# Kernel tuning notes

Hardware: AMD Instinct MI355X
Metric: run time of the kernel (lower is better)

Reference implementation:

```python
import jax, jax.numpy as jnp
import numpy as np

EMBED = 512
HEADS = 8
HD = EMBED // HEADS  # 64
LAYERS = 4
VOCAB = 16
SDIM = 3
TDEPTH = 8
BATCH = 2
SEQ = 1024
FF = 4 * EMBED
EPS = 1e-6      # fast-transformers CausalLinearAttention eps
LN_EPS = 1e-5   # torch LayerNorm default


def layer_norm(x, g, b):
    m = jnp.mean(x, axis=-1, keepdims=True)
    v = jnp.mean((x - m) ** 2, axis=-1, keepdims=True)
    return (x - m) * jax.lax.rsqrt(v + LN_EPS) * g + b


def setup_inputs() -> dict:
    key = jax.random.key(0)
    ks = iter(jax.random.split(key, 64))
    def nrm(shape, scale=0.02):
        return jax.random.normal(next(ks), shape, jnp.float32) * scale
    inp = {}
    inp['value'] = jax.random.randint(next(ks), (BATCH, SEQ), 0, VOCAB + 1)
    inp['depth'] = jax.random.randint(next(ks), (BATCH, SEQ), 0, TDEPTH + 1)
    inp['pos'] = jax.random.randint(next(ks), (SDIM, BATCH, SEQ), 0, 2 ** TDEPTH + 1)
    inp['sos'] = jax.random.normal(next(ks), (EMBED,), jnp.float32)
    # embeddings with padding_idx=0 -> zero row 0
    inp['tok_emb'] = nrm((VOCAB + 1, EMBED), 1.0).at[0].set(0.0)
    inp['depth_emb'] = nrm((TDEPTH + 1, EMBED), 1.0).at[0].set(0.0)
    inp['spatial_emb'] = nrm((SDIM, 2 ** TDEPTH + 1, EMBED), 1.0).at[:, 0].set(0.0)
    # per-layer stacked params (weights stored [in, out])
    for nm in ('Wq', 'Wk', 'Wv', 'Wo'):
        inp[nm] = nrm((LAYERS, EMBED, EMBED))
    for nm in ('bq', 'bk', 'bv', 'bo'):
        inp[nm] = jnp.zeros((LAYERS, EMBED), jnp.float32)
    inp['ln1_g'] = jnp.ones((LAYERS, EMBED), jnp.float32)
    inp['ln1_b'] = jnp.zeros((LAYERS, EMBED), jnp.float32)
    inp['ln2_g'] = jnp.ones((LAYERS, EMBED), jnp.float32)
    inp['ln2_b'] = jnp.zeros((LAYERS, EMBED), jnp.float32)
    inp['W1'] = nrm((LAYERS, EMBED, FF))
    inp['b1'] = jnp.zeros((LAYERS, FF), jnp.float32)
    inp['W2'] = nrm((LAYERS, FF, EMBED))
    inp['b2'] = jnp.zeros((LAYERS, EMBED), jnp.float32)
    inp['lnf_g'] = jnp.ones((EMBED,), jnp.float32)
    inp['lnf_b'] = jnp.zeros((EMBED,), jnp.float32)
    inp['Wh'] = nrm((EMBED, VOCAB + 1))
    return inp


def reference(value, depth, pos, sos, tok_emb, depth_emb, spatial_emb,
              Wq, bq, Wk, bk, Wv, bv, Wo, bo,
              ln1_g, ln1_b, ln2_g, ln2_b, W1, b1, W2, b2,
              lnf_g, lnf_b, Wh):
    N, S = value.shape
    # embedding sum
    x = tok_emb[value] + depth_emb[depth]
    for a in range(SDIM):
        x = x + spatial_emb[a][pos[a]]
    # shift right, prepend SOS
    x = jnp.concatenate([jnp.broadcast_to(sos, (N, 1, EMBED)), x[:, :-1, :]], axis=1)
    kmask = (value != 0).astype(x.dtype)  # (N,S) length mask applied to keys
    for i in range(LAYERS):
        # causal-linear attention (elu+1 feature map)
        q = jax.nn.elu((x @ Wq[i] + bq[i]).reshape(N, S, HEADS, HD)) + 1.0
        k = jax.nn.elu((x @ Wk[i] + bk[i]).reshape(N, S, HEADS, HD)) + 1.0
        v = (x @ Wv[i] + bv[i]).reshape(N, S, HEADS, HD)
        k = k * kmask[:, :, None, None]
        kv = jnp.cumsum(jnp.einsum('nshd,nshm->nshdm', k, v), axis=1)  # prefix K^T V state
        num = jnp.einsum('nshd,nshdm->nshm', q, kv)
        z = 1.0 / (jnp.einsum('nshd,nshd->nsh', q, jnp.cumsum(k, axis=1)) + EPS)
        attn = (num * z[..., None]).reshape(N, S, EMBED) @ Wo[i] + bo[i]
        # post-norm transformer block (fast-transformers TransformerEncoderLayer)
        x = layer_norm(x + attn, ln1_g[i], ln1_b[i])
        y = jax.nn.gelu(x @ W1[i] + b1[i], approximate=False) @ W2[i] + b2[i]
        x = layer_norm(x + y, ln2_g[i], ln2_b[i])
    x = layer_norm(x, lnf_g, lnf_b)  # encoder final norm
    return x @ Wh  # (N, S, num_vocab+1)
```

## Files before the change

kernel.cpp:

```cpp
#include <hip/hip_runtime.h>
#include <math.h>

#define EMB 512
#define SEQL 1024
#define NBATCH 2
#define NHEAD 8
#define FFDIM 2048
#define NLAYER 4
#define NROWS (NBATCH*SEQL)
#define CHUNK 128
#define NCH (SEQL/CHUNK)
#define QSTR 1536
#define LN_EPS_F 1e-5f
#define ATT_EPS_F 1e-6f

typedef __bf16 bf16x8 __attribute__((ext_vector_type(8)));
typedef float f32x4 __attribute__((ext_vector_type(4)));

__device__ __forceinline__ unsigned short f2bf(float f) {
    unsigned int u = __float_as_uint(f);
    u += 0x7FFFu + ((u >> 16) & 1u);
    return (unsigned short)(u >> 16);
}
__device__ __forceinline__ float bf2f(unsigned short x) {
    return __uint_as_float(((unsigned int)x) << 16);
}
__device__ __forceinline__ void gl_lds16(const unsigned short* g, unsigned short* l) {
    __builtin_amdgcn_global_load_lds(
        (__attribute__((address_space(1))) void*)const_cast<unsigned short*>(g),
        (__attribute__((address_space(3))) void*)l, 16, 0, 0);
}

__global__ void k_embed(const int* __restrict__ value, const int* __restrict__ depth,
                        const int* __restrict__ pos, const float* __restrict__ sos,
                        const float* __restrict__ tok, const float* __restrict__ dep,
                        const float* __restrict__ spa, float* __restrict__ X,
                        unsigned short* __restrict__ Xb) {
    int row = blockIdx.x;
    int n = row / SEQL, s = row % SEQL;
    int e = threadIdx.x * 4;
    float4 o;
    if (s == 0) {
        o = *(const float4*)(sos + e);
    } else {
        int sp = s - 1;
        int tv = value[n*SEQL + sp];
        int dv = depth[n*SEQL + sp];
        float4 a = *(const float4*)(tok + (size_t)tv*EMB + e);
        float4 b = *(const float4*)(dep + (size_t)dv*EMB + e);
        o.x = a.x+b.x; o.y = a.y+b.y; o.z = a.z+b.z; o.w = a.w+b.w;
#pragma unroll
        for (int ax = 0; ax < 3; ++ax) {
            int p = pos[((size_t)ax*NBATCH + n)*SEQL + sp];
            float4 c = *(const float4*)(spa + ((size_t)ax*257 + p)*EMB + e);
            o.x += c.x; o.y += c.y; o.z += c.z; o.w += c.w;
        }
    }
    *(float4*)(X + (size_t)row*EMB + e) = o;
    ushort4 ob; ob.x = f2bf(o.x); ob.y = f2bf(o.y); ob.z = f2bf(o.z); ob.w = f2bf(o.w);
    *(ushort4*)(Xb + (size_t)row*EMB + e) = ob;
}

__global__ __launch_bounds__(256) void k_wconv(
        const float* __restrict__ Wq0, const float* __restrict__ Wk0, const float* __restrict__ Wv0,
        const float* __restrict__ Wo0, const float* __restrict__ W10, const float* __restrict__ W20,
        const float* __restrict__ bq0, const float* __restrict__ bk0, const float* __restrict__ bv0,
        unsigned short* __restrict__ wAll, float* __restrict__ bqkv) {
    int idx = blockIdx.x*256 + threadIdx.x;
    if (idx >= 1572864) {
        int t = idx - 1572864;
        if (t < 6144) {
            int L = t / 1536, c = t % 1536;
            float v = (c < 512) ? bq0[L*512 + c] : (c < 1024) ? bk0[L*512 + c - 512] : bv0[L*512 + c - 1024];
            bqkv[L*1536 + c] = v;
        }
        return;
    }
    int L = idx / 393216;
    int t0 = idx % 393216;
    const float* Wq = Wq0 + (size_t)L*EMB*EMB;
    const float* Wk = Wk0 + (size_t)L*EMB*EMB;
    const float* Wv = Wv0 + (size_t)L*EMB*EMB;
    const float* Wo = Wo0 + (size_t)L*EMB*EMB;
    const float* W1 = W10 + (size_t)L*EMB*FFDIM;
    const float* W2 = W20 + (size_t)L*FFDIM*EMB;
    unsigned short* lay = wAll + (size_t)L*3145728;
    unsigned short* qkvT = lay;
    unsigned short* woT  = lay + 786432;
    unsigned short* w1T  = lay + 1048576;
    unsigned short* w2T  = lay + 2097152;

    const float* src; unsigned short* dst; size_t soff; size_t doff;
    if (t0 < 131072) {
        int sub = t0 >> 15, t = t0 & 32767;
        int kb = t >> 9, n = t & 511;
        src = (sub == 0) ? Wq : (sub == 1) ? Wk : (sub == 2) ? Wv : Wo;
        soff = (size_t)kb*8*512 + n;
        if (sub < 3) { dst = qkvT; doff = ((size_t)kb*1536 + sub*512 + n)*8; }
        else         { dst = woT;  doff = ((size_t)kb*512 + n)*8; }
        unsigned int p[4];
#pragma unroll
        for (int t2 = 0; t2 < 4; ++t2) {
            unsigned int lo = f2bf(src[soff + (size_t)(2*t2)*512]);
            unsigned int hi = f2bf(src[soff + (size_t)(2*t2+1)*512]);
            p[t2] = lo | (hi << 16);
        }
        *(uint4*)(dst + doff) = make_uint4(p[0], p[1], p[2], p[3]);
    } else if (t0 < 262144) {
        int t = t0 - 131072;
        int kb = t >> 11, n = t & 2047;
        soff = (size_t)kb*8*2048 + n;
        doff = ((size_t)kb*2048 + n)*8;
        unsigned int p[4];
#pragma unroll
        for (int t2 = 0; t2 < 4; ++t2) {
            unsigned int lo = f2bf(W1[soff + (size_t)(2*t2)*2048]);
            unsigned int hi = f2bf(W1[soff + (size_t)(2*t2+1)*2048]);
            p[t2] = lo | (hi << 16);
        }
        *(uint4*)(w1T + doff) = make_uint4(p[0], p[1], p[2], p[3]);
    } else {
        int t = t0 - 262144;
        int kb = t >> 9, n = t & 511;
        soff = (size_t)kb*8*512 + n;
        doff = ((size_t)kb*512 + n)*8;
        unsigned int p[4];
#pragma unroll
        for (int t2 = 0; t2 < 4; ++t2) {
            unsigned int lo = f2bf(W2[soff + (size_t)(2*t2)*512]);
            unsigned int hi = f2bf(W2[soff + (size_t)(2*t2+1)*512]);
            p[t2] = lo | (hi << 16);
        }
        *(uint4*)(w2T + doff) = make_uint4(p[0], p[1], p[2], p[3]);
    }
}

template<int BM, int BN, int WR, int WC, int ACT, int KS>
__global__ __launch_bounds__(WR*WC*64) void k_mgemm(
        const unsigned short* __restrict__ A, const unsigned short* __restrict__ Wt,
        const float* __restrict__ bias, const int* __restrict__ maskv,
        float* __restrict__ Cf, unsigned short* __restrict__ Cb,
        int N, int K, int lda, int ldc) {
    constexpr int THREADS = WR*WC*64;
    constexpr int WM = BM/WR, WN = BN/WC;
    constexpr int FM = WM/16, FN = WN/16;
    __shared__ __align__(16) unsigned short As[BM*32];
    __shared__ __align__(16) unsigned short Bs[BN*32];
    int tid = threadIdx.x;
    int lane = tid & 63;
    int l15 = lane & 15, lg = lane >> 4;
    int wid = tid >> 6;
    int wm = (wid / WC) * WM, wn = (wid % WC) * WN;
    int bm = blockIdx.y * BM, bn = blockIdx.x * BN;
    int kz = blockIdx.z;
    int ksl = K / KS;
    int kbeg = kz * ksl, kend = kbeg + ksl;

    f32x4 acc[FM][FN] = {};

    int a_off = (wm + l15)*32 + lg*8;
    int b_off = lg*BN*8 + (wn + l15)*8;

    for (int k0 = kbeg; k0 < kend; k0 += 32) {
#pragma unroll
        for (int i = 0; i < BM*4/THREADS; ++i) {
            int s = tid + i*THREADS;
            int m = s >> 2, kq = s & 3;
            gl_lds16(A + (size_t)(bm + m)*lda + k0 + kq*8, &As[s*8]);
        }
#pragma unroll
        for (int i = 0; i < BN*4/THREADS; ++i) {
            int s = tid + i*THREADS;
            int kb = s / BN, n = s - kb*BN;
            gl_lds16(Wt + ((size_t)(k0/8 + kb)*N + bn + n)*8, &Bs[s*8]);
        }
        __syncthreads();
        bf16x8 af[FM], bfr[FN];
#pragma unroll
        for (int mi = 0; mi < FM; ++mi) af[mi] = *(const bf16x8*)&As[a_off + mi*512];
#pragma unroll
        for (int ni = 0; ni < FN; ++ni) bfr[ni] = *(const bf16x8*)&Bs[b_off + ni*128];
#pragma unroll
        for (int mi = 0; mi < FM; ++mi)
#pragma unroll
            for (int ni = 0; ni < FN; ++ni)
                acc[mi][ni] = __builtin_amdgcn_mfma_f32_16x16x32_bf16(af[mi], bfr[ni], acc[mi][ni], 0, 0, 0);
        __syncthreads();
    }

    int r0 = bm + wm + lg*4;
    int c0 = bn + wn + l15;
    float* Cfz = Cf + (size_t)kz * 1048576;
#pragma unroll
    for (int mi = 0; mi < FM; ++mi) {
#pragma unroll
        for (int ni = 0; ni < FN; ++ni) {
            int col = c0 + ni*16;
#pragma unroll
            for (int j = 0; j < 4; ++j) {
                int row = r0 + mi*16 + j;
                float c = acc[mi][ni][j];
                if (KS == 1 || kz == 0) c += bias[col];
                if (ACT == 4) {
                    int reg = col >> 9;
                    if (reg == 0) { c = (c > 0.f) ? c + 1.f : expf(c); }
                    else if (reg == 1) { c = (c > 0.f) ? c + 1.f : expf(c); c *= (maskv[row] != 0) ? 1.f : 0.f; }
                    Cb[(size_t)row*ldc + col] = f2bf(c);
                } else if (ACT == 3) {
                    c = 0.5f * c * (1.f + erff(c * 0.70710678118654752f));
                    Cb[(size_t)row*ldc + col] = f2bf(c);
                } else {
                    Cfz[(size_t)row*ldc + col] = c;
                }
            }
        }
    }
}

__global__ __launch_bounds__(256) void k_cpart(
        const unsigned short* __restrict__ QKVb, float* __restrict__ Mpart, float* __restrict__ Upart) {
    int b = blockIdx.x;
    int c = b % NCH, h = (b / NCH) % NHEAD, n = b / (NCH * NHEAD);
    const unsigned short* Kp = QKVb + (size_t)(n*SEQL + c*CHUNK)*QSTR + 512 + h*64;
    const unsigned short* Vp = Kp + 512;
    __shared__ float Ks[8][64], Vs[8][64];
    int tid = threadIdx.x;
    int dk = tid >> 2, dv0 = (tid & 3) * 16;
    int lr = tid >> 5, lc = (tid & 31) * 2;
    float acc[16] = {};
    float uacc = 0.f;
    for (int s0 = 0; s0 < CHUNK; s0 += 8) {
        ushort2 k2 = *(const ushort2*)(Kp + (size_t)(s0 + lr)*QSTR + lc);
        ushort2 v2 = *(const ushort2*)(Vp + (size_t)(s0 + lr)*QSTR + lc);
        Ks[lr][lc] = bf2f(k2.x); Ks[lr][lc+1] = bf2f(k2.y);
        Vs[lr][lc] = bf2f(v2.x); Vs[lr][lc+1] = bf2f(v2.y);
        __syncthreads();
#pragma unroll
        for (int ss = 0; ss < 8; ++ss) {
            float kk = Ks[ss][dk];
#pragma unroll
            for (int j = 0; j < 16; ++j) acc[j] += kk * Vs[ss][dv0 + j];
        }
        if (tid < 64) {
#pragma unroll
            for (int ss = 0; ss < 8; ++ss) uacc += Ks[ss][tid];
        }
        __syncthreads();
    }
    size_t base = ((size_t)(n*NHEAD + h)*NCH + c) * 4096;
#pragma unroll
    for (int j = 0; j < 16; ++j) Mpart[base + (size_t)dk*64 + dv0 + j] = acc[j];
    if (tid < 64) Upart[((size_t)(n*NHEAD + h)*NCH + c)*64 + tid] = uacc;
}

__global__ __launch_bounds__(512) void k_cattend(
        const unsigned short* __restrict__ QKVb, const float* __restrict__ Mpart,
        const float* __restrict__ Upart, unsigned short* __restrict__ Ab) {
    int b = blockIdx.x;
    int c = b % NCH, h = (b / NCH) % NHEAD, n = b / (NCH * NHEAD);
    int nh = n*NHEAD + h;
    int tid = threadIdx.x;
    int wid = tid >> 6, lane = tid & 63;
    int l15 = lane & 15, lg = lane >> 4;
    __shared__ __align__(16) unsigned short Vt[64*200];
    __shared__ __align__(16) unsigned short St[11264];
    __shared__ float wf[64];
    int rowbase = n*SEQL + c*CHUNK;

    {
        int j = tid & 127, vd0 = (tid >> 7) * 16;
        const unsigned short* vp = QKVb + (size_t)(rowbase + j)*QSTR + 1024 + h*64 + vd0;
        uint4 u0 = *(const uint4*)vp;
        uint4 u1 = *(const uint4*)(vp + 8);
        const unsigned short* e0 = (const unsigned short*)&u0;
        const unsigned short* e1 = (const unsigned short*)&u1;
#pragma unroll
        for (int t = 0; t < 8; ++t) Vt[(vd0 + t)*200 + j] = e0[t];
#pragma unroll
        for (int t = 0; t < 8; ++t) Vt[(vd0 + 8 + t)*200 + j] = e1[t];
    }
    {
        int d = tid & 63, vd0 = (tid >> 6) * 8;
        float pr[8] = {};
        for (int cc = 0; cc < c; ++cc) {
            const float* pp = Mpart + ((size_t)nh*NCH + cc)*4096 + (size_t)d*64 + vd0;
            float4 p0 = *(const float4*)pp;
            float4 p1 = *(const float4*)(pp + 4);
            pr[0]+=p0.x; pr[1]+=p0.y; pr[2]+=p0.z; pr[3]+=p0.w;
            pr[4]+=p1.x; pr[5]+=p1.y; pr[6]+=p1.z; pr[7]+=p1.w;
        }
#pragma unroll
        for (int t = 0; t < 8; ++t) Vt[(vd0 + t)*200 + 128 + d] = f2bf(pr[t]);
    }
    if (tid < 64) {
        float u = 0.f;
        for (int cc = 0; cc < c; ++cc) u += Upart[((size_t)nh*NCH + cc)*64 + tid];
        wf[tid] = u;
    }

    int r0 = wid * 16;
    int koff = lg * 8;
    const unsigned short* qp = QKVb + (size_t)(rowbase + r0 + l15)*QSTR + h*64 + koff;
    uint4 uq0 = *(const uint4*)qp;
    uint4 uq1 = *(const uint4*)(qp + 32);
    bf16x8 aq0 = *(bf16x8*)&uq0;
    bf16x8 aq1 = *(bf16x8*)&uq1;

    int nact = (wid & ~1) + 2;
    int sstr_ = 32*((wid >> 1) + 1) + 8;
    int p_ = wid >> 1;
    int sig = p_*(p_+1) + (wid & 1)*(p_+1);
    int stoff_ = 128*wid + 512*sig;

    float rsum[4] = {0.f, 0.f, 0.f, 0.f};
    for (int nt = 0; nt < nact; ++nt) {
        int j0 = nt*16;
        const unsigned short* kp = QKVb + (size_t)(rowbase + j0 + l15)*QSTR + 512 + h*64 + koff;
        uint4 uk0 = *(const uint4*)kp;
        uint4 uk1 = *(const uint4*)(kp + 32);
        f32x4 s = {0.f, 0.f, 0.f, 0.f};
        s = __builtin_amdgcn_mfma_f32_16x16x32_bf16(aq0, *(bf16x8*)&uk0, s, 0, 0, 0);
        s = __builtin_amdgcn_mfma_f32_16x16x32_bf16(aq1, *(bf16x8*)&uk1, s, 0, 0, 0);
        int jcol = j0 + l15;
#pragma unroll
        for (int r = 0; r < 4; ++r) {
            int irow = r0 + lg*4 + r;
            float sv = (jcol <= irow) ? s[r] : 0.f;
            rsum[r] += sv;
            St[stoff_ + (lg*4 + r)*sstr_ + jcol] = f2bf(sv);
        }
    }
    __syncthreads();

    float qw = 0.f;
    const unsigned short* q0e = (const unsigned short*)&uq0;
    const unsigned short* q1e = (const unsigned short*)&uq1;
#pragma unroll
    for (int jj = 0; jj < 8; ++jj) {
        qw += bf2f(q0e[jj]) * wf[koff + jj];
        qw += bf2f(q1e[jj]) * wf[32 + koff + jj];
    }
    qw += __shfl_xor(qw, 16);
    qw += __shfl_xor(qw, 32);

    f32x4 o[4] = {};
    int nkr = (wid >> 1) + 1;
    for (int ks = 0; ks < nkr; ++ks) {
        bf16x8 as = *(bf16x8*)&St[stoff_ + l15*sstr_ + ks*32 + koff];
#pragma unroll
        for (int nt = 0; nt < 4; ++nt) {
            bf16x8 bv = *(bf16x8*)&Vt[(nt*16 + l15)*200 + ks*32 + koff];
            o[nt] = __builtin_amdgcn_mfma_f32_16x16x32_bf16(as, bv, o[nt], 0, 0, 0);
        }
    }
#pragma unroll
    for (int kk = 0; kk < 2; ++kk) {
        bf16x8 as = kk ? aq1 : aq0;
#pragma unroll
        for (int nt = 0; nt < 4; ++nt) {
            bf16x8 bv = *(bf16x8*)&Vt[(nt*16 + l15)*200 + 128 + kk*32 + koff];
            o[nt] = __builtin_amdgcn_mfma_f32_16x16x32_bf16(as, bv, o[nt], 0, 0, 0);
        }
    }

#pragma unroll
    for (int r = 0; r < 4; ++r) {
        float v = rsum[r];
        v += __shfl_xor(v, 1); v += __shfl_xor(v, 2);
        v += __shfl_xor(v, 4); v += __shfl_xor(v, 8);
        rsum[r] = v;
    }
#pragma unroll
    for (int r = 0; r < 4; ++r) {
        float qwr = __shfl(qw, lg*4 + r);
        float z = 1.f / (rsum[r] + qwr + ATT_EPS_F);
        int orow = rowbase + r0 + lg*4 + r;
        unsigned short* op = Ab + (size_t)orow*EMB + h*64 + l15;
#pragma unroll
        for (int nt = 0; nt < 4; ++nt)
            op[nt*16] = f2bf(o[nt][r] * z);
    }
}

__global__ __launch_bounds__(256) void k_ln(
        const float* __restrict__ X, const float* __restrict__ R, int nsl,
        const float* __restrict__ g, const float* __restrict__ bb,
        float* __restrict__ Y, unsigned short* __restrict__ Yb) {
    int row = blockIdx.x, tid = threadIdx.x;
    float2 v = *(const float2*)(X + (size_t)row*EMB + tid*2);
    for (int z = 0; z < nsl; ++z) {
        float2 r = *(const float2*)(R + (size_t)z*1048576 + (size_t)row*EMB + tid*2);
        v.x += r.x; v.y += r.y;
    }
    float s = v.x + v.y, ss = v.x*v.x + v.y*v.y;
#pragma unroll
    for (int off = 32; off; off >>= 1) {
        s  += __shfl_down(s, off);
        ss += __shfl_down(ss, off);
    }
    __shared__ float sb[4], ssb[4];
    int wid = tid >> 6, lane = tid & 63;
    if (!lane) { sb[wid] = s; ssb[wid] = ss; }
    __syncthreads();
    float tot  = sb[0] + sb[1] + sb[2] + sb[3];
    float tots = ssb[0] + ssb[1] + ssb[2] + ssb[3];
    float mean = tot * (1.f/EMB);
    float var  = tots * (1.f/EMB) - mean*mean;
    float inv  = rsqrtf(var + LN_EPS_F);
    int e = tid*2;
    float2 o;
    o.x = (v.x - mean)*inv*g[e]   + bb[e];
    o.y = (v.y - mean)*inv*g[e+1] + bb[e+1];
    *(float2*)(Y + (size_t)row*EMB + e) = o;
    ushort2 ob; ob.x = f2bf(o.x); ob.y = f2bf(o.y);
    *(ushort2*)(Yb + (size_t)row*EMB + e) = ob;
}

__global__ __launch_bounds__(256) void k_lnhead(
        const float* __restrict__ X, const float* __restrict__ g, const float* __restrict__ bb,
        const float* __restrict__ Wh, float* __restrict__ out) {
    __shared__ float ys[8][512];
    __shared__ float whs[512*17];
    int tid = threadIdx.x;
    for (int i = tid; i < 512*17; i += 256) whs[i] = Wh[i];

    int row = tid >> 5, l32 = tid & 31;
    int rg = blockIdx.x * 8 + row;
    const float* xr = X + (size_t)rg*EMB + l32*16;
    float v[16];
    float s = 0.f, ss = 0.f;
#pragma unroll
    for (int i = 0; i < 4; ++i) {
        float4 a = *(const float4*)(xr + i*4);
        v[i*4+0]=a.x; v[i*4+1]=a.y; v[i*4+2]=a.z; v[i*4+3]=a.w;
        s += a.x+a.y+a.z+a.w;
        ss += a.x*a.x+a.y*a.y+a.z*a.z+a.w*a.w;
    }
#pragma unroll
    for (int off = 1; off < 32; off <<= 1) { s += __shfl_xor(s, off); ss += __shfl_xor(ss, off); }
    float mean = s * (1.f/EMB);
    float var  = ss * (1.f/EMB) - mean*mean;
    float inv  = rsqrtf(var + LN_EPS_F);
    int c0 = l32*16;
#pragma unroll
    for (int i = 0; i < 16; ++i) {
        float y = (v[i] - mean)*inv*g[c0+i] + bb[c0+i];
        ys[row][c0+i] = y;
    }
    __syncthreads();

    float part[17];
#pragma unroll
    for (int cc = 0; cc < 17; ++cc) part[cc] = 0.f;
    for (int kk = 0; kk < 16; ++kk) {
        int k = c0 + kk;
        float yv = ys[row][k];
#pragma unroll
        for (int cc = 0; cc < 17; ++cc) part[cc] += yv * whs[k*17 + cc];
    }
#pragma unroll
    for (int cc = 0; cc < 17; ++cc) {
        float pv = part[cc];
#pragma unroll
        for (int off = 1; off < 32; off <<= 1) pv += __shfl_xor(pv, off);
        if (l32 == 0) out[(size_t)rg*17 + cc] = pv;
    }
}

extern "C" void kernel_launch(void* const* d_in, const int* in_sizes, int n_in,
                              void* d_out, int out_size, void* d_ws, size_t ws_size,
                              hipStream_t stream) {
    (void)in_sizes; (void)n_in; (void)out_size; (void)ws_size;
    const int*   value = (const int*)d_in[0];
    const int*   depth = (const int*)d_in[1];
    const int*   pos   = (const int*)d_in[2];
    const float* sos   = (const float*)d_in[3];
    const float* tok   = (const float*)d_in[4];
    const float* dep   = (const float*)d_in[5];
    const float* spa   = (const float*)d_in[6];
    const float* Wq0   = (const float*)d_in[7];
    const float* Wk0   = (const float*)d_in[8];
    const float* Wv0   = (const float*)d_in[9];
    const float* Wo0   = (const float*)d_in[10];
    const float* bq0   = (const float*)d_in[11];
    const float* bk0   = (const float*)d_in[12];
    const float* bv0   = (const float*)d_in[13];
    const float* bo0   = (const float*)d_in[14];
    const float* ln1g  = (const float*)d_in[15];
    const float* ln1b  = (const float*)d_in[16];
    const float* ln2g  = (const float*)d_in[17];
    const float* ln2b  = (const float*)d_in[18];
    const float* W10   = (const float*)d_in[19];
    const float* b10   = (const float*)d_in[20];
    const float* W20   = (const float*)d_in[21];
    const float* b20   = (const float*)d_in[22];
    const float* lnfg  = (const float*)d_in[23];
    const float* lnfb  = (const float*)d_in[24];
    const float* Wh    = (const float*)d_in[25];
    float* out = (float*)d_out;
    float* ws  = (float*)d_ws;

    float*          X     = ws;
    unsigned short* Xb    = (unsigned short*)(ws + 1048576);
    unsigned short* QKVb  = (unsigned short*)(ws + 1572864);
    unsigned short* Ab    = (unsigned short*)(ws + 3145728);
    unsigned short* Hb    = (unsigned short*)(ws + 1572864);
    float*          Mpart = ws + 3670016;
    float*          Upart = ws + 4194304;
    float*          AO    = ws + 4202496;
    float*          bqkv  = ws + 8396800;
    unsigned short* wAll  = (unsigned short*)(ws + 8402944);

    k_embed<<<NROWS, 128, 0, stream>>>(value, depth, pos, sos, tok, dep, spa, X, Xb);
    k_wconv<<<6168, 256, 0, stream>>>(Wq0, Wk0, Wv0, Wo0, W10, W20, bq0, bk0, bv0, wAll, bqkv);

    for (int L = 0; L < NLAYER; ++L) {
        unsigned short* lay  = wAll + (size_t)L*3145728;
        unsigned short* qkvT = lay;
        unsigned short* woT  = lay + 786432;
        unsigned short* w1T  = lay + 1048576;
        unsigned short* w2T  = lay + 2097152;

        k_mgemm<64,128,2,2,4,1><<<dim3(12,32), 256, 0, stream>>>(
            Xb, qkvT, bqkv + L*1536, value, nullptr, QKVb, 1536, 512, 512, 1536);

        k_cpart<<<NBATCH*NHEAD*NCH, 256, 0, stream>>>(QKVb, Mpart, Upart);
        k_cattend<<<NBATCH*NHEAD*NCH, 512, 0, stream>>>(QKVb, Mpart, Upart, Ab);

        k_mgemm<64,64,2,2,0,2><<<dim3(8,32,2), 256, 0, stream>>>(
            Ab, woT, bo0 + (size_t)L*EMB, nullptr, AO, nullptr, 512, 512, 512, 512);
        k_ln<<<NROWS, 256, 0, stream>>>(X, AO, 2, ln1g + (size_t)L*EMB, ln1b + (size_t)L*EMB, X, Xb);

        k_mgemm<64,128,2,2,3,1><<<dim3(16,32), 256, 0, stream>>>(
            Xb, w1T, b10 + (size_t)L*FFDIM, nullptr, nullptr, Hb, 2048, 512, 512, 2048);

        k_mgemm<64,64,2,2,0,4><<<dim3(8,32,4), 256, 0, stream>>>(
            Hb, w2T, b20 + (size_t)L*EMB, nullptr, AO, nullptr, 512, 2048, 2048, 512);
        k_ln<<<NROWS, 256, 0, stream>>>(X, AO, 4, ln2g + (size_t)L*EMB, ln2b + (size_t)L*EMB, X, Xb);
    }
    k_lnhead<<<NROWS/8, 256, 0, stream>>>(X, lnfg, lnfb, Wh, out);
}
```

Measured before the change: 424.4 us.

## Split chunked linear-attention kernels into two blocks per chunk for more parallelism

Both the chunk-partial kernel and the attend kernel now launch twice as many blocks. The partial kernel splits each 128-row chunk into two 64-row halves, and the attend kernel splits its 8 waves into two 256-thread blocks of 4 waves each. With only 128 blocks before, the GPU's compute units were underused. In exchange, each attend block redundantly loads the full V tile and sums twice as many prefix partials, Mpart and Upart grow, and the workspace offsets shift to fit.

```diff
diff --git a/kernel.cpp b/kernel.cpp
--- a/kernel.cpp
+++ b/kernel.cpp
@@ -220,8 +220,12 @@
 __global__ __launch_bounds__(256) void k_cpart(
         const unsigned short* __restrict__ QKVb, float* __restrict__ Mpart, float* __restrict__ Upart) {
     int b = blockIdx.x;
-    int c = b % NCH, h = (b / NCH) % NHEAD, n = b / (NCH * NHEAD);
-    const unsigned short* Kp = QKVb + (size_t)(n*SEQL + c*CHUNK)*QSTR + 512 + h*64;
+    int half = b & 1;
+    int cidx = b >> 1;
+    int c = cidx % NCH;
+    int nh = cidx / NCH;
+    int h = nh % NHEAD, n = nh / NHEAD;
+    const unsigned short* Kp = QKVb + (size_t)(n*SEQL + c*CHUNK + half*64)*QSTR + 512 + h*64;
     const unsigned short* Vp = Kp + 512;
     __shared__ float Ks[8][64], Vs[8][64];
     int tid = threadIdx.x;
@@ -229,7 +233,7 @@
     int lr = tid >> 5, lc = (tid & 31) * 2;
     float acc[16] = {};
     float uacc = 0.f;
-    for (int s0 = 0; s0 < CHUNK; s0 += 8) {
+    for (int s0 = 0; s0 < 64; s0 += 8) {
         ushort2 k2 = *(const ushort2*)(Kp + (size_t)(s0 + lr)*QSTR + lc);
         ushort2 v2 = *(const ushort2*)(Vp + (size_t)(s0 + lr)*QSTR + lc);
         Ks[lr][lc] = bf2f(k2.x); Ks[lr][lc+1] = bf2f(k2.y);
@@ -247,20 +251,24 @@
         }
         __syncthreads();
     }
-    size_t base = ((size_t)(n*NHEAD + h)*NCH + c) * 4096;
+    size_t base = (size_t)b * 4096;
 #pragma unroll
     for (int j = 0; j < 16; ++j) Mpart[base + (size_t)dk*64 + dv0 + j] = acc[j];
-    if (tid < 64) Upart[((size_t)(n*NHEAD + h)*NCH + c)*64 + tid] = uacc;
-}
-
-__global__ __launch_bounds__(512) void k_cattend(
+    if (tid < 64) Upart[(size_t)b*64 + tid] = uacc;
+}
+
+__global__ __launch_bounds__(256) void k_cattend(
         const unsigned short* __restrict__ QKVb, const float* __restrict__ Mpart,
         const float* __restrict__ Upart, unsigned short* __restrict__ Ab) {
     int b = blockIdx.x;
-    int c = b % NCH, h = (b / NCH) % NHEAD, n = b / (NCH * NHEAD);
-    int nh = n*NHEAD + h;
+    int grp = b & 1;
+    int cidx = b >> 1;
+    int c = cidx % NCH;
+    int nh = cidx / NCH;
+    int h = nh % NHEAD, n = nh / NHEAD;
     int tid = threadIdx.x;
-    int wid = tid >> 6, lane = tid & 63;
+    int wid = (grp << 2) + (tid >> 6);
+    int lane = tid & 63;
     int l15 = lane & 15, lg = lane >> 4;
     __shared__ __align__(16) unsigned short Vt[64*200];
     __shared__ __align__(16) unsigned short St[11264];
@@ -268,33 +276,41 @@
     int rowbase = n*SEQL + c*CHUNK;
 
     {
-        int j = tid & 127, vd0 = (tid >> 7) * 16;
-        const unsigned short* vp = QKVb + (size_t)(rowbase + j)*QSTR + 1024 + h*64 + vd0;
-        uint4 u0 = *(const uint4*)vp;
-        uint4 u1 = *(const uint4*)(vp + 8);
-        const unsigned short* e0 = (const unsigned short*)&u0;
-        const unsigned short* e1 = (const unsigned short*)&u1;
-#pragma unroll
-        for (int t = 0; t < 8; ++t) Vt[(vd0 + t)*200 + j] = e0[t];
-#pragma unroll
-        for (int t = 0; t < 8; ++t) Vt[(vd0 + 8 + t)*200 + j] = e1[t];
+        int j = tid & 127;
+        const unsigned short* vp = QKVb + (size_t)(rowbase + j)*QSTR + 1024 + h*64;
+#pragma unroll
+        for (int vh = 0; vh < 2; ++vh) {
+            int vd0 = (tid >> 7) * 16 + vh * 32;
+            uint4 u0 = *(const uint4*)(vp + vd0);
+            uint4 u1 = *(const uint4*)(vp + vd0 + 8);
+            const unsigned short* e0 = (const unsigned short*)&u0;
+            const unsigned short* e1 = (const unsigned short*)&u1;
+#pragma unroll
+            for (int t = 0; t < 8; ++t) Vt[(vd0 + t)*200 + j] = e0[t];
+#pragma unroll
+            for (int t = 0; t < 8; ++t) Vt[(vd0 + 8 + t)*200 + j] = e1[t];
+        }
     }
     {
-        int d = tid & 63, vd0 = (tid >> 6) * 8;
-        float pr[8] = {};
-        for (int cc = 0; cc < c; ++cc) {
-            const float* pp = Mpart + ((size_t)nh*NCH + cc)*4096 + (size_t)d*64 + vd0;
-            float4 p0 = *(const float4*)pp;
-            float4 p1 = *(const float4*)(pp + 4);
-            pr[0]+=p0.x; pr[1]+=p0.y; pr[2]+=p0.z; pr[3]+=p0.w;
-            pr[4]+=p1.x; pr[5]+=p1.y; pr[6]+=p1.z; pr[7]+=p1.w;
-        }
-#pragma unroll
-        for (int t = 0; t < 8; ++t) Vt[(vd0 + t)*200 + 128 + d] = f2bf(pr[t]);
+        int d = tid & 63;
+#pragma unroll
+        for (int ph = 0; ph < 2; ++ph) {
+            int vd0 = (tid >> 6) * 8 + ph * 32;
+            float pr[8] = {};
+            for (int p = 0; p < 2*c; ++p) {
+                const float* pp = Mpart + ((size_t)nh*NCH*2 + p)*4096 + (size_t)d*64 + vd0;
+                float4 p0 = *(const float4*)pp;
+                float4 p1 = *(const float4*)(pp + 4);
+                pr[0]+=p0.x; pr[1]+=p0.y; pr[2]+=p0.z; pr[3]+=p0.w;
+                pr[4]+=p1.x; pr[5]+=p1.y; pr[6]+=p1.z; pr[7]+=p1.w;
+            }
+#pragma unroll
+            for (int t = 0; t < 8; ++t) Vt[(vd0 + t)*200 + 128 + d] = f2bf(pr[t]);
+        }
     }
     if (tid < 64) {
         float u = 0.f;
-        for (int cc = 0; cc < c; ++cc) u += Upart[((size_t)nh*NCH + cc)*64 + tid];
+        for (int p = 0; p < 2*c; ++p) u += Upart[((size_t)nh*NCH*2 + p)*64 + tid];
         wf[tid] = u;
     }
 
@@ -506,10 +522,10 @@
     unsigned short* Ab    = (unsigned short*)(ws + 3145728);
     unsigned short* Hb    = (unsigned short*)(ws + 1572864);
     float*          Mpart = ws + 3670016;
-    float*          Upart = ws + 4194304;
-    float*          AO    = ws + 4202496;
-    float*          bqkv  = ws + 8396800;
-    unsigned short* wAll  = (unsigned short*)(ws + 8402944);
+    float*          Upart = ws + 4718592;
+    float*          AO    = ws + 4734976;
+    float*          bqkv  = ws + 8929280;
+    unsigned short* wAll  = (unsigned short*)(ws + 8935424);
 
     k_embed<<<NROWS, 128, 0, stream>>>(value, depth, pos, sos, tok, dep, spa, X, Xb);
     k_wconv<<<6168, 256, 0, stream>>>(Wq0, Wk0, Wv0, Wo0, W10, W20, bq0, bk0, bv0, wAll, bqkv);
@@ -524,8 +540,8 @@
         k_mgemm<64,128,2,2,4,1><<<dim3(12,32), 256, 0, stream>>>(
             Xb, qkvT, bqkv + L*1536, value, nullptr, QKVb, 1536, 512, 512, 1536);
 
-        k_cpart<<<NBATCH*NHEAD*NCH, 256, 0, stream>>>(QKVb, Mpart, Upart);
-        k_cattend<<<NBATCH*NHEAD*NCH, 512, 0, stream>>>(QKVb, Mpart, Upart, Ab);
+        k_cpart<<<NBATCH*NHEAD*NCH*2, 256, 0, stream>>>(QKVb, Mpart, Upart);
+        k_cattend<<<NBATCH*NHEAD*NCH*2, 256, 0, stream>>>(QKVb, Mpart, Upart, Ab);
 
         k_mgemm<64,64,2,2,0,2><<<dim3(8,32,2), 256, 0, stream>>>(
             Ab, woT, bo0 + (size_t)L*EMB, nullptr, AO, nullptr, 512, 512, 512, 512);
```

After: 430.6 us. Within noise of the previous version (+1.5%).

## Triple-buffer GEMM LDS tiles with async global-to-LDS prefetch pipeline

Applied to the files above, without the earlier changes.

Reworks the MFMA GEMM main loop into a three-stage software pipeline. Two K-tiles ahead are issued with global_load_lds into rotating LDS buffers, and explicit vmcnt waits plus raw s_barrier replace the __syncthreads pairs. The goal is to hide global memory latency behind MFMA compute. It triples LDS usage, which may lower occupancy, and it depends on hand-counted vmcnt values that only work for certain NL values and assume nt >= 2.

```diff
diff --git a/kernel.cpp b/kernel.cpp
--- a/kernel.cpp
+++ b/kernel.cpp
@@ -29,6 +29,13 @@
     __builtin_amdgcn_global_load_lds(
         (__attribute__((address_space(1))) void*)const_cast<unsigned short*>(g),
         (__attribute__((address_space(3))) void*)l, 16, 0, 0);
+}
+template<int N_> __device__ __forceinline__ void wait_vm() {
+    if constexpr (N_ == 0) asm volatile("s_waitcnt vmcnt(0)" ::: "memory");
+    else if constexpr (N_ == 2) asm volatile("s_waitcnt vmcnt(2)" ::: "memory");
+    else if constexpr (N_ == 3) asm volatile("s_waitcnt vmcnt(3)" ::: "memory");
+    else if constexpr (N_ == 4) asm volatile("s_waitcnt vmcnt(4)" ::: "memory");
+    else if constexpr (N_ == 6) asm volatile("s_waitcnt vmcnt(6)" ::: "memory");
 }
 
 __global__ void k_embed(const int* __restrict__ value, const int* __restrict__ depth,
@@ -144,8 +151,11 @@
     constexpr int THREADS = WR*WC*64;
     constexpr int WM = BM/WR, WN = BN/WC;
     constexpr int FM = WM/16, FN = WN/16;
-    __shared__ __align__(16) unsigned short As[BM*32];
-    __shared__ __align__(16) unsigned short Bs[BN*32];
+    constexpr int AL = BM*4/THREADS;
+    constexpr int BL = BN*4/THREADS;
+    constexpr int NL = AL + BL;
+    __shared__ __align__(16) unsigned short As[3][BM*32];
+    __shared__ __align__(16) unsigned short Bs[3][BN*32];
     int tid = threadIdx.x;
     int lane = tid & 63;
     int l15 = lane & 15, lg = lane >> 4;
@@ -154,39 +164,63 @@
     int bm = blockIdx.y * BM, bn = blockIdx.x * BN;
     int kz = blockIdx.z;
     int ksl = K / KS;
-    int kbeg = kz * ksl, kend = kbeg + ksl;
+    int kbeg = kz * ksl;
+    int nt = ksl / 32;
 
     f32x4 acc[FM][FN] = {};
 
     int a_off = (wm + l15)*32 + lg*8;
     int b_off = lg*BN*8 + (wn + l15)*8;
 
-    for (int k0 = kbeg; k0 < kend; k0 += 32) {
-#pragma unroll
-        for (int i = 0; i < BM*4/THREADS; ++i) {
+    auto stage = [&](int buf, int ks) {
+        int k0 = kbeg + ks*32;
+#pragma unroll
+        for (int i = 0; i < AL; ++i) {
             int s = tid + i*THREADS;
             int m = s >> 2, kq = s & 3;
-            gl_lds16(A + (size_t)(bm + m)*lda + k0 + kq*8, &As[s*8]);
-        }
-#pragma unroll
-        for (int i = 0; i < BN*4/THREADS; ++i) {
+            gl_lds16(A + (size_t)(bm + m)*lda + k0 + kq*8, &As[buf][s*8]);
+        }
+#pragma unroll
+        for (int i = 0; i < BL; ++i) {
             int s = tid + i*THREADS;
             int kb = s / BN, n = s - kb*BN;
-            gl_lds16(Wt + ((size_t)(k0/8 + kb)*N + bn + n)*8, &Bs[s*8]);
-        }
-        __syncthreads();
+            gl_lds16(Wt + ((size_t)(k0/8 + kb)*N + bn + n)*8, &Bs[buf][s*8]);
+        }
+    };
+    auto compute = [&](int buf) {
         bf16x8 af[FM], bfr[FN];
 #pragma unroll
-        for (int mi = 0; mi < FM; ++mi) af[mi] = *(const bf16x8*)&As[a_off + mi*512];
-#pragma unroll
-        for (int ni = 0; ni < FN; ++ni) bfr[ni] = *(const bf16x8*)&Bs[b_off + ni*128];
+        for (int mi = 0; mi < FM; ++mi) af[mi] = *(const bf16x8*)&As[buf][a_off + mi*512];
+#pragma unroll
+        for (int ni = 0; ni < FN; ++ni) bfr[ni] = *(const bf16x8*)&Bs[buf][b_off + ni*128];
 #pragma unroll
         for (int mi = 0; mi < FM; ++mi)
 #pragma unroll
             for (int ni = 0; ni < FN; ++ni)
                 acc[mi][ni] = __builtin_amdgcn_mfma_f32_16x16x32_bf16(af[mi], bfr[ni], acc[mi][ni], 0, 0, 0);
-        __syncthreads();
-    }
+    };
+
+    stage(0, 0);
+    stage(1, 1);
+    for (int t = 0; t < nt - 2; ++t) {
+        stage((t + 2) % 3, t + 2);
+        wait_vm<2*NL>();
+        __builtin_amdgcn_s_barrier();
+        __builtin_amdgcn_sched_barrier(0);
+        compute(t % 3);
+        __builtin_amdgcn_sched_barrier(0);
+        __builtin_amdgcn_s_barrier();
+    }
+    wait_vm<NL>();
+    __builtin_amdgcn_s_barrier();
+    __builtin_amdgcn_sched_barrier(0);
+    compute((nt - 2) % 3);
+    __builtin_amdgcn_sched_barrier(0);
+    __builtin_amdgcn_s_barrier();
+    wait_vm<0>();
+    __builtin_amdgcn_s_barrier();
+    __builtin_amdgcn_sched_barrier(0);
+    compute((nt - 1) % 3);
 
     int r0 = bm + wm + lg*4;
     int c0 = bn + wn + l15;
```

Measured after the change: 417.9 us. Within noise of the previous version (-1.5%).
